# Performance work log

Hardware: AMD Instinct MI355X
Metric: run time of the kernel (lower is better)

Reference implementation:

```python
import jax, jax.numpy as jnp
import numpy as np


def setup_inputs() -> dict:
    key = jax.random.key(0)
    x = jax.random.normal(key, (16, 2048, 64), dtype=jnp.float32)
    return {"x": x, "pred_len": 720, "k": 16, "low_freq": 1}


def reference(x, pred_len, k, low_freq):
    # x: (b, t, d); t assumed even (matches torch branch x_freq[:, low_freq:-1])
    b, t, d = x.shape
    x_freq = jnp.fft.rfft(x, axis=1)[:, low_freq:-1]          # (b, F, d) complex
    f = jnp.fft.rfftfreq(t).astype(jnp.float32)[low_freq:-1]  # (F,)

    # top-k frequencies per (batch, channel) by magnitude
    mag = jnp.transpose(jnp.abs(x_freq), (0, 2, 1))           # (b, d, F)
    _, idx = jax.lax.top_k(mag, k)                            # (b, d, k)
    xf_sel = jnp.take_along_axis(jnp.transpose(x_freq, (0, 2, 1)), idx, axis=2)
    xf_sel = jnp.transpose(xf_sel, (0, 2, 1))                 # (b, k, d)
    f_sel = jnp.transpose(f[idx], (0, 2, 1))                  # (b, k, d)

    # extrapolate: append conjugate / negated-frequency pairs
    xf = jnp.concatenate([xf_sel, jnp.conj(xf_sel)], axis=1)  # (b, 2k, d)
    ff = jnp.concatenate([f_sel, -f_sel], axis=1)[:, :, None, :]   # (b, 2k, 1, d)
    t_val = jnp.arange(t + pred_len, dtype=jnp.float32)[None, None, :, None]
    amp = (jnp.abs(xf) / t)[:, :, None, :]                    # (b, 2k, 1, d)
    phase = jnp.angle(xf)[:, :, None, :]                      # (b, 2k, 1, d)
    x_time = amp * jnp.cos(2.0 * jnp.pi * ff * t_val + phase) # (b, 2k, t+pred_len, d)
    return x_time.sum(axis=1)                                 # (b, t+pred_len, d)
```

## Files before the change

### kernel.cpp

```cpp
#include <hip/hip_runtime.h>
#include <hip/hip_bf16.h>

#define B_SZ 16
#define T_SZ 2048
#define D_SZ 64
#define M_SZ 1024
#define K_SEL 16
#define TOUT 2768
#define TCHUNK 4
#define NCHUNK (TOUT / TCHUNK)

__global__ __launch_bounds__(256) void fft_topk_kernel(
    const float* __restrict__ x,
    int* __restrict__ sel_j,
    float* __restrict__ sel_re,
    float* __restrict__ sel_im)
{
    __shared__ float a_re[M_SZ], a_im[M_SZ];
    __shared__ float tw_re[M_SZ / 2], tw_im[M_SZ / 2];
    __shared__ float X_re[M_SZ], X_im[M_SZ];
    __shared__ float mag2[M_SZ];
    __shared__ float wmax[4];
    __shared__ int   warg[4];
    __shared__ int   sel_list[K_SEL];

    const int bd  = blockIdx.x;
    const int b   = bd >> 6;
    const int d   = bd & 63;
    const int tid = threadIdx.x;

    for (int k = tid; k < M_SZ / 2; k += 256) {
        float a = (float)k * (1.0f / 512.0f);
        tw_re[k] =  cospif(a);
        tw_im[k] = -sinpif(a);
    }

    const float* xb = x + (size_t)b * T_SZ * D_SZ + d;
    for (int m = tid; m < M_SZ; m += 256) {
        float xe = xb[(2 * m) * D_SZ];
        float xo = xb[(2 * m + 1) * D_SZ];
        int pos = __brev((unsigned)m) >> 22;
        a_re[pos] = xe;
        a_im[pos] = xo;
    }
    __syncthreads();

    for (int s = 0; s < 10; ++s) {
        #pragma unroll 2
        for (int q = tid; q < M_SZ / 2; q += 256) {
            int half = 1 << s;
            int pos  = q & (half - 1);
            int i0   = ((q >> s) << (s + 1)) + pos;
            int i1   = i0 + half;
            int twi  = pos << (9 - s);
            float wr = tw_re[twi], wi = tw_im[twi];
            float br = a_re[i1],  bi = a_im[i1];
            float tr = fmaf(wr, br, -wi * bi);
            float ti = fmaf(wr, bi,  wi * br);
            float ar = a_re[i0],  ai = a_im[i0];
            a_re[i0] = ar + tr;  a_im[i0] = ai + ti;
            a_re[i1] = ar - tr;  a_im[i1] = ai - ti;
        }
        __syncthreads();
    }

    for (int j = tid; j < M_SZ; j += 256) {
        if (j == 0) {
            X_re[0] = 0.0f; X_im[0] = 0.0f; mag2[0] = -2.0f;
            continue;
        }
        int jc = M_SZ - j;
        float zr = a_re[j],  zi = a_im[j];
        float cr = a_re[jc], ci = a_im[jc];
        float er = 0.5f * (zr + cr), ei = 0.5f * (zi - ci);
        float ur = zr - cr,  vv = zi + ci;
        float orr = 0.5f * vv, oii = -0.5f * ur;
        float a  = (float)j * (1.0f / 1024.0f);
        float twr =  cospif(a);
        float twq = -sinpif(a);
        float xr = er + twr * orr - twq * oii;
        float xi = ei + twr * oii + twq * orr;
        X_re[j] = xr; X_im[j] = xi;
        mag2[j] = xr * xr + xi * xi;
    }
    __syncthreads();

    const int lane = tid & 63, wv = tid >> 6;
    for (int it = 0; it < K_SEL; ++it) {
        float bv = -1.0f; int bj = M_SZ;
        #pragma unroll
        for (int r = 0; r < 4; ++r) {
            int j = tid + 256 * r;
            float v = mag2[j];
            if (v > bv) { bv = v; bj = j; }
        }
        #pragma unroll
        for (int off = 32; off; off >>= 1) {
            float ov = __shfl_xor(bv, off);
            int   oj = __shfl_xor(bj, off);
            if (ov > bv || (ov == bv && oj < bj)) { bv = ov; bj = oj; }
        }
        if (lane == 0) { wmax[wv] = bv; warg[wv] = bj; }
        __syncthreads();
        if (tid == 0) {
            float best = wmax[0]; int bidx = warg[0];
            #pragma unroll
            for (int w = 1; w < 4; ++w) {
                if (wmax[w] > best || (wmax[w] == best && warg[w] < bidx)) {
                    best = wmax[w]; bidx = warg[w];
                }
            }
            sel_list[it] = bidx;
            mag2[bidx] = -2.0f;
        }
        __syncthreads();
    }

    if (tid < K_SEL) {
        int j = sel_list[tid];
        sel_j [bd * K_SEL + tid] = j;
        sel_re[bd * K_SEL + tid] = X_re[j];
        sel_im[bd * K_SEL + tid] = X_im[j];
    }
}

__global__ __launch_bounds__(256) void synth_kernel(
    const int*   __restrict__ sel_j,
    const float* __restrict__ sel_re,
    const float* __restrict__ sel_im,
    float* __restrict__ out)
{
    __shared__ int   js [K_SEL][65];
    __shared__ float res[K_SEL][65];
    __shared__ float ims[K_SEL][65];

    const int bid   = blockIdx.x;
    const int b     = bid / NCHUNK;
    const int chunk = bid - b * NCHUNK;
    const int tid   = threadIdx.x;

    for (int i = tid; i < D_SZ * K_SEL; i += 256) {
        int d = i >> 4, q = i & 15;
        int g = (b * D_SZ + d) * K_SEL + q;
        js [q][d] = sel_j [g];
        res[q][d] = sel_re[g];
        ims[q][d] = sel_im[g];
    }
    __syncthreads();

    const int d   = tid & 63;
    const int tau = chunk * TCHUNK + (tid >> 6);

    float acc = 0.0f;
    #pragma unroll
    for (int q = 0; q < K_SEL; ++q) {
        int   j  = js[q][d];
        int   ph = (j * tau) & (T_SZ - 1);
        float r  = (float)ph * (1.0f / (float)T_SZ);
        float c  = __builtin_amdgcn_cosf(r);
        float s  = __builtin_amdgcn_sinf(r);
        acc = fmaf(res[q][d], c, acc);
        acc = fmaf(-ims[q][d], s, acc);
    }
    out[((size_t)b * TOUT + tau) * D_SZ + d] = acc * (1.0f / 1024.0f);
}

extern "C" void kernel_launch(void* const* d_in, const int* in_sizes, int n_in,
                              void* d_out, int out_size, void* d_ws, size_t ws_size,
                              hipStream_t stream) {
    const float* x = (const float*)d_in[0];

    int*   sel_j  = (int*)d_ws;
    float* sel_re = (float*)((char*)d_ws + (size_t)B_SZ * D_SZ * K_SEL * 4);
    float* sel_im = (float*)((char*)d_ws + (size_t)2 * B_SZ * D_SZ * K_SEL * 4);

    fft_topk_kernel<<<dim3(B_SZ * D_SZ), dim3(256), 0, stream>>>(
        x, sel_j, sel_re, sel_im);

    synth_kernel<<<dim3(B_SZ * NCHUNK), dim3(256), 0, stream>>>(
        sel_j, sel_re, sel_im, (float*)d_out);
}
```

Baseline: 116.0 us.

## Pre-transpose input, warp-local top-k merge, and register-resident multi-tau synthesis

Adds a tiled transpose kernel so each FFT block reads its (batch, channel) series contiguously as float2 rather than with a stride of 64 floats. Top-k selection now runs 16 rounds per warp entirely in registers with shuffles, followed by a single 64-candidate merge in warp 0, which removes the 32 block-wide barriers of the old loop. The synthesis kernel loads each thread's 16 selected frequencies into registers with vector loads and computes 8 output times per thread, dropping the shared staging and its barrier. The cost is an extra kernel launch plus a full write and re-read of a transposed copy of the input in workspace.

```diff
diff --git a/kernel.cpp b/kernel.cpp
--- a/kernel.cpp
+++ b/kernel.cpp
@@ -7,11 +7,34 @@
 #define M_SZ 1024
 #define K_SEL 16
 #define TOUT 2768
-#define TCHUNK 4
-#define NCHUNK (TOUT / TCHUNK)
+#define TPT 8
+#define TAUS_PER_BLOCK (4 * TPT)
+#define NCHUNK ((TOUT + TAUS_PER_BLOCK - 1) / TAUS_PER_BLOCK)
+
+__global__ __launch_bounds__(256) void transpose_kernel(
+    const float* __restrict__ x, float* __restrict__ xT)
+{
+    __shared__ float tile[64][65];
+    const int b    = blockIdx.y;
+    const int t0   = blockIdx.x * 64;
+    const int lane = threadIdx.x & 63;
+    const int row4 = threadIdx.x >> 6;
+
+    #pragma unroll
+    for (int rr = 0; rr < 16; ++rr) {
+        int r = rr * 4 + row4;
+        tile[r][lane] = x[((size_t)b * T_SZ + t0 + r) * D_SZ + lane];
+    }
+    __syncthreads();
+    #pragma unroll
+    for (int rr = 0; rr < 16; ++rr) {
+        int d = rr * 4 + row4;
+        xT[((size_t)b * D_SZ + d) * T_SZ + t0 + lane] = tile[lane][d];
+    }
+}
 
 __global__ __launch_bounds__(256) void fft_topk_kernel(
-    const float* __restrict__ x,
+    const float* __restrict__ xT,
     int* __restrict__ sel_j,
     float* __restrict__ sel_re,
     float* __restrict__ sel_im)
@@ -20,14 +43,13 @@
     __shared__ float tw_re[M_SZ / 2], tw_im[M_SZ / 2];
     __shared__ float X_re[M_SZ], X_im[M_SZ];
     __shared__ float mag2[M_SZ];
-    __shared__ float wmax[4];
-    __shared__ int   warg[4];
-    __shared__ int   sel_list[K_SEL];
-
-    const int bd  = blockIdx.x;
-    const int b   = bd >> 6;
-    const int d   = bd & 63;
-    const int tid = threadIdx.x;
+    __shared__ float cand_v[64];
+    __shared__ int   cand_j[64];
+
+    const int bd   = blockIdx.x;
+    const int tid  = threadIdx.x;
+    const int lane = tid & 63;
+    const int w    = tid >> 6;
 
     for (int k = tid; k < M_SZ / 2; k += 256) {
         float a = (float)k * (1.0f / 512.0f);
@@ -35,13 +57,14 @@
         tw_im[k] = -sinpif(a);
     }
 
-    const float* xb = x + (size_t)b * T_SZ * D_SZ + d;
-    for (int m = tid; m < M_SZ; m += 256) {
-        float xe = xb[(2 * m) * D_SZ];
-        float xo = xb[(2 * m + 1) * D_SZ];
+    const float2* xb2 = (const float2*)(xT + (size_t)bd * T_SZ);
+    #pragma unroll
+    for (int r = 0; r < 4; ++r) {
+        int m = tid + 256 * r;
+        float2 v = xb2[m];
         int pos = __brev((unsigned)m) >> 22;
-        a_re[pos] = xe;
-        a_im[pos] = xo;
+        a_re[pos] = v.x;
+        a_im[pos] = v.y;
     }
     __syncthreads();
 
@@ -85,42 +108,52 @@
     }
     __syncthreads();
 
-    const int lane = tid & 63, wv = tid >> 6;
+    float v[4]; int jj[4];
+    #pragma unroll
+    for (int r = 0; r < 4; ++r) {
+        jj[r] = w * 256 + r * 64 + lane;
+        v[r]  = mag2[jj[r]];
+    }
+    float my_v = -3.0f; int my_j = 0;
     for (int it = 0; it < K_SEL; ++it) {
-        float bv = -1.0f; int bj = M_SZ;
-        #pragma unroll
-        for (int r = 0; r < 4; ++r) {
-            int j = tid + 256 * r;
-            float v = mag2[j];
-            if (v > bv) { bv = v; bj = j; }
-        }
+        float bv = -2.5f; int bj = 1 << 20;
+        #pragma unroll
+        for (int r = 0; r < 4; ++r)
+            if (v[r] > bv) { bv = v[r]; bj = jj[r]; }
         #pragma unroll
         for (int off = 32; off; off >>= 1) {
             float ov = __shfl_xor(bv, off);
             int   oj = __shfl_xor(bj, off);
             if (ov > bv || (ov == bv && oj < bj)) { bv = ov; bj = oj; }
         }
-        if (lane == 0) { wmax[wv] = bv; warg[wv] = bj; }
-        __syncthreads();
-        if (tid == 0) {
-            float best = wmax[0]; int bidx = warg[0];
+        if (lane == it) { my_v = bv; my_j = bj; }
+        #pragma unroll
+        for (int r = 0; r < 4; ++r)
+            if (jj[r] == bj) v[r] = -2.0f;
+    }
+    if (lane < K_SEL) { cand_v[w * K_SEL + lane] = my_v; cand_j[w * K_SEL + lane] = my_j; }
+    __syncthreads();
+
+    if (w == 0) {
+        float cv = cand_v[lane]; int cj = cand_j[lane];
+        int out_j = 0;
+        for (int it = 0; it < K_SEL; ++it) {
+            float rv = cv; int rj = cj;
             #pragma unroll
-            for (int w = 1; w < 4; ++w) {
-                if (wmax[w] > best || (wmax[w] == best && warg[w] < bidx)) {
-                    best = wmax[w]; bidx = warg[w];
-                }
+            for (int off = 32; off; off >>= 1) {
+                float ov = __shfl_xor(rv, off);
+                int   oj = __shfl_xor(rj, off);
+                if (ov > rv || (ov == rv && oj < rj)) { rv = ov; rj = oj; }
             }
-            sel_list[it] = bidx;
-            mag2[bidx] = -2.0f;
-        }
-        __syncthreads();
-    }
-
-    if (tid < K_SEL) {
-        int j = sel_list[tid];
-        sel_j [bd * K_SEL + tid] = j;
-        sel_re[bd * K_SEL + tid] = X_re[j];
-        sel_im[bd * K_SEL + tid] = X_im[j];
+            if (lane == it) out_j = rj;
+            if (cj == rj) cv = -2.0f;
+        }
+        if (lane < K_SEL) {
+            int j = out_j;
+            sel_j [bd * K_SEL + lane] = j;
+            sel_re[bd * K_SEL + lane] = X_re[j];
+            sel_im[bd * K_SEL + lane] = X_im[j];
+        }
     }
 }
 
@@ -130,39 +163,47 @@
     const float* __restrict__ sel_im,
     float* __restrict__ out)
 {
-    __shared__ int   js [K_SEL][65];
-    __shared__ float res[K_SEL][65];
-    __shared__ float ims[K_SEL][65];
-
     const int bid   = blockIdx.x;
     const int b     = bid / NCHUNK;
     const int chunk = bid - b * NCHUNK;
     const int tid   = threadIdx.x;
-
-    for (int i = tid; i < D_SZ * K_SEL; i += 256) {
-        int d = i >> 4, q = i & 15;
-        int g = (b * D_SZ + d) * K_SEL + q;
-        js [q][d] = sel_j [g];
-        res[q][d] = sel_re[g];
-        ims[q][d] = sel_im[g];
-    }
-    __syncthreads();
-
-    const int d   = tid & 63;
-    const int tau = chunk * TCHUNK + (tid >> 6);
-
-    float acc = 0.0f;
-    #pragma unroll
-    for (int q = 0; q < K_SEL; ++q) {
-        int   j  = js[q][d];
-        int   ph = (j * tau) & (T_SZ - 1);
-        float r  = (float)ph * (1.0f / (float)T_SZ);
-        float c  = __builtin_amdgcn_cosf(r);
-        float s  = __builtin_amdgcn_sinf(r);
-        acc = fmaf(res[q][d], c, acc);
-        acc = fmaf(-ims[q][d], s, acc);
-    }
-    out[((size_t)b * TOUT + tau) * D_SZ + d] = acc * (1.0f / 1024.0f);
+    const int d     = tid & 63;
+    const int tg    = tid >> 6;
+
+    const int g = (b * D_SZ + d) * K_SEL;
+    int   j [K_SEL];
+    float re[K_SEL];
+    float im[K_SEL];
+    const int4*   pj = (const int4*)  (sel_j  + g);
+    const float4* pr = (const float4*)(sel_re + g);
+    const float4* pi = (const float4*)(sel_im + g);
+    #pragma unroll
+    for (int r = 0; r < 4; ++r) {
+        int4   a = pj[r];
+        float4 c = pr[r];
+        float4 s = pi[r];
+        j [4*r+0] = a.x; j [4*r+1] = a.y; j [4*r+2] = a.z; j [4*r+3] = a.w;
+        re[4*r+0] = c.x; re[4*r+1] = c.y; re[4*r+2] = c.z; re[4*r+3] = c.w;
+        im[4*r+0] = s.x; im[4*r+1] = s.y; im[4*r+2] = s.z; im[4*r+3] = s.w;
+    }
+
+    const int tau0 = chunk * TAUS_PER_BLOCK + tg * TPT;
+    #pragma unroll
+    for (int u = 0; u < TPT; ++u) {
+        int tau = tau0 + u;
+        if (tau >= TOUT) break;
+        float acc = 0.0f;
+        #pragma unroll
+        for (int q = 0; q < K_SEL; ++q) {
+            int   ph = (j[q] * tau) & (T_SZ - 1);
+            float r  = (float)ph * (1.0f / (float)T_SZ);
+            float c  = __builtin_amdgcn_cosf(r);
+            float s  = __builtin_amdgcn_sinf(r);
+            acc = fmaf(re[q], c, acc);
+            acc = fmaf(-im[q], s, acc);
+        }
+        out[((size_t)b * TOUT + tau) * D_SZ + d] = acc * (1.0f / 1024.0f);
+    }
 }
 
 extern "C" void kernel_launch(void* const* d_in, const int* in_sizes, int n_in,
@@ -170,12 +211,16 @@
                               hipStream_t stream) {
     const float* x = (const float*)d_in[0];
 
-    int*   sel_j  = (int*)d_ws;
-    float* sel_re = (float*)((char*)d_ws + (size_t)B_SZ * D_SZ * K_SEL * 4);
-    float* sel_im = (float*)((char*)d_ws + (size_t)2 * B_SZ * D_SZ * K_SEL * 4);
+    float* xT     = (float*)d_ws;
+    char*  base   = (char*)d_ws + (size_t)B_SZ * T_SZ * D_SZ * 4;
+    int*   sel_j  = (int*)base;
+    float* sel_re = (float*)(base + (size_t)B_SZ * D_SZ * K_SEL * 4);
+    float* sel_im = (float*)(base + (size_t)2 * B_SZ * D_SZ * K_SEL * 4);
+
+    transpose_kernel<<<dim3(T_SZ / 64, B_SZ), dim3(256), 0, stream>>>(x, xT);
 
     fft_topk_kernel<<<dim3(B_SZ * D_SZ), dim3(256), 0, stream>>>(
-        x, sel_j, sel_re, sel_im);
+        xT, sel_j, sel_re, sel_im);
 
     synth_kernel<<<dim3(B_SZ * NCHUNK), dim3(256), 0, stream>>>(
         sel_j, sel_re, sel_im, (float*)d_out);
```

After: 117.2 us. About the same (+1.0%).
